# Kernel tuning notes

Hardware: AMD Instinct MI355X
Metric: run time of the kernel (lower is better)

## Reference

```python
import jax, jax.numpy as jnp
import numpy as np

EPS = 1e-8
Q_MAX = 127.0  # 2**(8-1) - 1


def _activation_quant(x):
    gamma = jnp.maximum(jnp.max(jnp.abs(x)), EPS)
    scale = Q_MAX / gamma
    x_int = jnp.clip(jnp.round(x * scale), -Q_MAX, Q_MAX)
    x_fq = x_int / scale
    # straight-through estimator
    return x + jax.lax.stop_gradient(x_fq - x)


def _weight_quant(w):
    gamma = jnp.maximum(jnp.mean(jnp.abs(w)), EPS)
    w_int = jnp.clip(jnp.round(w / gamma), -1.0, 1.0)
    w_fq = w_int * gamma
    return w + jax.lax.stop_gradient(w_fq - w)


def setup_inputs() -> dict:
    key = jax.random.key(0)
    kx, kw, kb = jax.random.split(key, 3)
    in_features, out_features = 2048, 2048
    x = jax.random.normal(kx, (4, 4096, in_features), dtype=jnp.float32)
    # nn.Linear default init: U(-1/sqrt(fan_in), 1/sqrt(fan_in))
    bound = 1.0 / np.sqrt(in_features)
    W = jax.random.uniform(kw, (out_features, in_features), dtype=jnp.float32,
                           minval=-bound, maxval=bound)
    b = jax.random.uniform(kb, (out_features,), dtype=jnp.float32,
                           minval=-bound, maxval=bound)
    return {"x": x, "W": W, "b": b}


def reference(x, W, b):
    x_q = _activation_quant(x)          # int8 absmax fake-quant
    w_q = _weight_quant(W)              # ternary {-g, 0, g} fake-quant
    # F.linear: x @ W^T + b
    return jnp.einsum('bsi,oi->bso', x_q, w_q) + b
```

## Files before the change

### kernel.cpp

```cpp
#include <hip/hip_runtime.h>
#include <hip/hip_bf16.h>
#include <stdint.h>

typedef __attribute__((ext_vector_type(4))) int i32x4;

static constexpr long M_ = 16384;
static constexpr long N_ = 2048;
static constexpr long K_ = 2048;


#define GLOAD_LDS16(g, l)                                                          \
  __builtin_amdgcn_global_load_lds(                                               \
      (const __attribute__((address_space(1))) unsigned int*)(g),                 \
      (__attribute__((address_space(3))) unsigned int*)(l), 16, 0, 0)

__global__ __launch_bounds__(256) void k_stats(const float4* __restrict__ x,
                                               const float4* __restrict__ w,
                                               unsigned* __restrict__ gx_bits,
                                               double* __restrict__ gw_sum) {
  const int b = blockIdx.x;
  const int lane = threadIdx.x & 63, wv = threadIdx.x >> 6;
  if (b < 2048) {
    const long S = 524288;
    long i = (long)b * 256 + threadIdx.x;
    float m0 = 0.f, m1 = 0.f;
#pragma unroll
    for (int it = 0; it < 8; ++it) {
      float4 v0 = x[i];
      float4 v1 = x[i + S];
      m0 = fmaxf(m0, fmaxf(fmaxf(fabsf(v0.x), fabsf(v0.y)), fmaxf(fabsf(v0.z), fabsf(v0.w))));
      m1 = fmaxf(m1, fmaxf(fmaxf(fabsf(v1.x), fabsf(v1.y)), fmaxf(fabsf(v1.z), fabsf(v1.w))));
      i += 2 * S;
    }
    float m = fmaxf(m0, m1);
#pragma unroll
    for (int off = 32; off > 0; off >>= 1) m = fmaxf(m, __shfl_down(m, off));
    __shared__ float sm[4];
    if (lane == 0) sm[wv] = m;
    __syncthreads();
    if (threadIdx.x == 0) {
      float bm = fmaxf(fmaxf(sm[0], sm[1]), fmaxf(sm[2], sm[3]));
      atomicMax(gx_bits, __float_as_uint(bm));
    }
  } else {
    const long S = 131072;
    long i = (long)(b - 2048) * 256 + threadIdx.x;
    double s = 0.0;
#pragma unroll
    for (int it = 0; it < 8; ++it) {
      float4 v = w[i];
      s += (double)fabsf(v.x) + (double)fabsf(v.y) + (double)fabsf(v.z) + (double)fabsf(v.w);
      i += S;
    }
#pragma unroll
    for (int off = 32; off > 0; off >>= 1) s += __shfl_down(s, off);
    __shared__ double sd[4];
    if (lane == 0) sd[wv] = s;
    __syncthreads();
    if (threadIdx.x == 0) atomicAdd(gw_sum, (sd[0] + sd[1]) + (sd[2] + sd[3]));
  }
}

__global__ __launch_bounds__(256) void k_quant(const float4* __restrict__ x,
                                               const float4* __restrict__ w,
                                               char4* __restrict__ xq,
                                               char4* __restrict__ wq,
                                               const unsigned* __restrict__ gx_bits,
                                               const double* __restrict__ gw_sum) {
  const int b = blockIdx.x;
  if (b < 2048) {
    const double gx = (double)fmaxf(__uint_as_float(*gx_bits), 1e-8f);
    const double scale = 127.0 / gx;
    const long S = 524288;
    long i = (long)b * 256 + threadIdx.x;
#pragma unroll
    for (int it = 0; it < 16; ++it) {
      float4 v = x[i];
      char4 o;
      o.x = (signed char)(int)fmin(fmax(rint((double)v.x * scale), -127.0), 127.0);
      o.y = (signed char)(int)fmin(fmax(rint((double)v.y * scale), -127.0), 127.0);
      o.z = (signed char)(int)fmin(fmax(rint((double)v.z * scale), -127.0), 127.0);
      o.w = (signed char)(int)fmin(fmax(rint((double)v.w * scale), -127.0), 127.0);
      xq[i] = o;
      i += S;
    }
  } else {
    const double gw = fmax(*gw_sum * (1.0 / 4194304.0), 1e-8);
    const double inv = 1.0 / gw;
    const long S = 131072;
    long i = (long)(b - 2048) * 256 + threadIdx.x;
#pragma unroll
    for (int it = 0; it < 8; ++it) {
      float4 v = w[i];
      char4 o;
      o.x = (signed char)(int)fmin(fmax(rint((double)v.x * inv), -1.0), 1.0);
      o.y = (signed char)(int)fmin(fmax(rint((double)v.y * inv), -1.0), 1.0);
      o.z = (signed char)(int)fmin(fmax(rint((double)v.z * inv), -1.0), 1.0);
      o.w = (signed char)(int)fmin(fmax(rint((double)v.w * inv), -1.0), 1.0);
      wq[i] = o;
      i += S;
    }
  }
}


template <int ISB, int BUF, int KS>
__device__ __forceinline__ void stage2(signed char* lds, const signed char* gp, int kb,
                                       int go0, int ldsl0) {
  constexpr int R = ISB * 65536 + BUF * 32768 + KS * 16384;
  GLOAD_LDS16(gp + kb + go0, lds + R + ldsl0);
  GLOAD_LDS16(gp + kb + go0 + 32768, lds + R + ldsl0 + 1024);
}

template <int BUF, int KS, int SGBUF, int SGKS>
__device__ __forceinline__ void pairphase(signed char* lds, const signed char* Ap,
                                          const signed char* Bp, int kb,
                                          const signed char* pA, const signed char* pB,
                                          int go0, int ldsl0, i32x4 acc[8][4]) {
  constexpr int RB = BUF * 32768 + KS * 16384;
  i32x4 b4[4], alo[4], ahi[4];
#pragma unroll
  for (int n = 0; n < 4; ++n) b4[n] = *(const i32x4*)(pB + RB + n * 1024);
#pragma unroll
  for (int m = 0; m < 4; ++m) alo[m] = *(const i32x4*)(pA + RB + m * 1024);
#pragma unroll
  for (int m = 0; m < 4; ++m) ahi[m] = *(const i32x4*)(pA + RB + 4096 + m * 1024);

  stage2<0, SGBUF, SGKS>(lds, Ap, kb, go0, ldsl0);
  stage2<1, SGBUF, SGKS>(lds, Bp, kb, go0, ldsl0);

  __builtin_amdgcn_s_barrier();
  __builtin_amdgcn_s_setprio(1);
#pragma unroll
  for (int m = 0; m < 4; ++m)
#pragma unroll
    for (int n = 0; n < 4; ++n)
      acc[m][n] = __builtin_amdgcn_mfma_i32_16x16x64_i8(alo[m], b4[n], acc[m][n], 0, 0, 0);
#pragma unroll
  for (int m = 0; m < 4; ++m)
#pragma unroll
    for (int n = 0; n < 4; ++n)
      acc[4 + m][n] =
          __builtin_amdgcn_mfma_i32_16x16x64_i8(ahi[m], b4[n], acc[4 + m][n], 0, 0, 0);
  __builtin_amdgcn_s_setprio(0);
  asm volatile("s_waitcnt vmcnt(8)" ::: "memory");
  __builtin_amdgcn_s_barrier();
  __builtin_amdgcn_sched_barrier(0);
}

__global__ __launch_bounds__(512, 2) void k_gemm(
    const signed char* __restrict__ Aq, const signed char* __restrict__ Bq,
    const float* __restrict__ bias, float* __restrict__ out,
    const unsigned* __restrict__ gx_bits, const double* __restrict__ gw_sum) {
  extern __shared__ signed char lds[];

  const int tid = threadIdx.x;
  const int lane = tid & 63;
  const int wid = tid >> 6;
  const int wave_m = wid >> 2;
  const int wave_n = wid & 3;
  const int l15 = lane & 15;

  const int wg = (int)((blockIdx.x & 7) * 64 + (blockIdx.x >> 3));
  const int nblk = wg & 7;
  const int mblk = wg >> 3;
  const long brow = (long)mblk * 256;
  const long bcol = (long)nblk * 256;

  const signed char* Ap = Aq + brow * K_;
  const signed char* Bp = Bq + bcol * K_;

  const int swz = ((lane >> 4) ^ ((l15 >> 1) & 3)) << 4;
  const signed char* pA = lds + (wave_m * 128 + l15) * 64 + swz;
  const signed char* pB = lds + 65536 + (wave_n * 64 + l15) * 64 + swz;

  const int c0 = (lane & 3) ^ ((lane >> 3) & 3);
  const int go0 = (wid * 32 + (lane >> 2)) * (int)K_ + c0 * 16;
  const int ldsl0 = wid * 2048;

  i32x4 acc[8][4];
#pragma unroll
  for (int m = 0; m < 8; m++)
#pragma unroll
    for (int n = 0; n < 4; n++) acc[m][n] = (i32x4){0, 0, 0, 0};

  stage2<0, 0, 0>(lds, Ap, 0, go0, ldsl0);
  stage2<1, 0, 0>(lds, Bp, 0, go0, ldsl0);
  stage2<0, 0, 1>(lds, Ap, 64, go0, ldsl0);
  stage2<1, 0, 1>(lds, Bp, 64, go0, ldsl0);
  stage2<0, 1, 0>(lds, Ap, 128, go0, ldsl0);
  stage2<1, 1, 0>(lds, Bp, 128, go0, ldsl0);
  asm volatile("s_waitcnt vmcnt(0)" ::: "memory");
  __builtin_amdgcn_s_barrier();

  for (int kt = 0; kt < (int)K_; kt += 256) {
    const int k1h = (kt + 192) & 2047;
    const int k2 = (kt + 256) & 2047;
    const int k3 = (kt + 384) & 2047;
    pairphase<0, 0, 1, 1>(lds, Ap, Bp, k1h, pA, pB, go0, ldsl0, acc);
    pairphase<0, 1, 0, 0>(lds, Ap, Bp, k2, pA, pB, go0, ldsl0, acc);
    pairphase<1, 0, 0, 1>(lds, Ap, Bp, k2 + 64, pA, pB, go0, ldsl0, acc);
    pairphase<1, 1, 1, 0>(lds, Ap, Bp, k3, pA, pB, go0, ldsl0, acc);
  }

  const float gxf = fmaxf(__uint_as_float(*gx_bits), 1e-8f);
  const double gwd = fmax(*gw_sum * (1.0 / 4194304.0), 1e-8);
  const float alpha = (float)((double)gxf * gwd * (1.0 / 127.0));

#pragma unroll
  for (int n = 0; n < 4; ++n) {
    const long col = bcol + wave_n * 64 + n * 16 + l15;
    const float bv = bias[col];
#pragma unroll
    for (int m = 0; m < 8; ++m) {
      const long row0 = brow + wave_m * 128 + m * 16 + (lane >> 4) * 4;
#pragma unroll
      for (int r = 0; r < 4; ++r) {
        out[(row0 + r) * N_ + col] = (float)acc[m][n][r] * alpha + bv;
      }
    }
  }
}

extern "C" void kernel_launch(void* const* d_in, const int* in_sizes, int n_in,
                              void* d_out, int out_size, void* d_ws, size_t ws_size,
                              hipStream_t stream) {
  const float* x = (const float*)d_in[0];
  const float* W = (const float*)d_in[1];
  const float* b = (const float*)d_in[2];
  float* out = (float*)d_out;

  char* ws = (char*)d_ws;
  double* gw_sum = (double*)ws;
  unsigned* gx_bits = (unsigned*)(ws + 8);
  signed char* xq = (signed char*)(ws + 256);
  signed char* wq = (signed char*)(ws + 256 + (size_t)M_ * (size_t)K_);

  static bool attr_set = false;
  if (!attr_set) {
    (void)hipFuncSetAttribute(reinterpret_cast<const void*>(&k_gemm),
                              hipFuncAttributeMaxDynamicSharedMemorySize, 131072);
    attr_set = true;
  }

  hipMemsetAsync(ws, 0, 16, stream);
  hipLaunchKernelGGL(k_stats, dim3(2560), dim3(256), 0, stream,
                     (const float4*)x, (const float4*)W, gx_bits, gw_sum);
  hipLaunchKernelGGL(k_quant, dim3(2560), dim3(256), 0, stream,
                     (const float4*)x, (const float4*)W, (char4*)xq, (char4*)wq,
                     gx_bits, gw_sum);
  hipLaunchKernelGGL(k_gemm, dim3((unsigned)((M_ / 256) * (N_ / 256))), dim3(512),
                     131072, stream, xq, wq, b, out, gx_bits, gw_sum);
}
```

Baseline: 155.7 us.

## Shrink GEMM tile to 128x256 with 4 waves and double-buffered LDS

The int8 GEMM moves from a 256x256 tile with 8 waves and 128 KB of LDS in a deep 4-slot pipeline to a 128x256 tile with 4 waves, 48 KB of LDS and a simple two-buffer scheme. A and B prefetches are split across the two MFMA halves of each k-step. The smaller LDS footprint and block should allow more resident workgroups and give a finer grid, at the cost of less operand reuse per tile and a full vmcnt(0) wait every k-step. The stats kernel also unrolls its absmax loop to four independent loads per iteration.

New measurement: 158.3 us. About the same (+1.6%).

```diff
diff --git a/kernel.cpp b/kernel.cpp
--- a/kernel.cpp
+++ b/kernel.cpp
@@ -23,16 +23,20 @@
   if (b < 2048) {
     const long S = 524288;
     long i = (long)b * 256 + threadIdx.x;
-    float m0 = 0.f, m1 = 0.f;
-#pragma unroll
-    for (int it = 0; it < 8; ++it) {
+    float m0 = 0.f, m1 = 0.f, m2 = 0.f, m3 = 0.f;
+#pragma unroll
+    for (int it = 0; it < 4; ++it) {
       float4 v0 = x[i];
       float4 v1 = x[i + S];
+      float4 v2 = x[i + 2 * S];
+      float4 v3 = x[i + 3 * S];
       m0 = fmaxf(m0, fmaxf(fmaxf(fabsf(v0.x), fabsf(v0.y)), fmaxf(fabsf(v0.z), fabsf(v0.w))));
       m1 = fmaxf(m1, fmaxf(fmaxf(fabsf(v1.x), fabsf(v1.y)), fmaxf(fabsf(v1.z), fabsf(v1.w))));
-      i += 2 * S;
-    }
-    float m = fmaxf(m0, m1);
+      m2 = fmaxf(m2, fmaxf(fmaxf(fabsf(v2.x), fabsf(v2.y)), fmaxf(fabsf(v2.z), fabsf(v2.w))));
+      m3 = fmaxf(m3, fmaxf(fmaxf(fabsf(v3.x), fabsf(v3.y)), fmaxf(fabsf(v3.z), fabsf(v3.w))));
+      i += 4 * S;
+    }
+    float m = fmaxf(fmaxf(m0, m1), fmaxf(m2, m3));
 #pragma unroll
     for (int off = 32; off > 0; off >>= 1) m = fmaxf(m, __shfl_down(m, off));
     __shared__ float sm[4];
@@ -104,51 +108,65 @@
 }
 
 
-template <int ISB, int BUF, int KS>
-__device__ __forceinline__ void stage2(signed char* lds, const signed char* gp, int kb,
-                                       int go0, int ldsl0) {
-  constexpr int R = ISB * 65536 + BUF * 32768 + KS * 16384;
-  GLOAD_LDS16(gp + kb + go0, lds + R + ldsl0);
-  GLOAD_LDS16(gp + kb + go0 + 32768, lds + R + ldsl0 + 1024);
-}
-
-template <int BUF, int KS, int SGBUF, int SGKS>
-__device__ __forceinline__ void pairphase(signed char* lds, const signed char* Ap,
-                                          const signed char* Bp, int kb,
-                                          const signed char* pA, const signed char* pB,
-                                          int go0, int ldsl0, i32x4 acc[8][4]) {
-  constexpr int RB = BUF * 32768 + KS * 16384;
-  i32x4 b4[4], alo[4], ahi[4];
+template <int BUF>
+__device__ __forceinline__ void stageA(signed char* lds, const signed char* gp, int kb,
+                                       int goA, int wslotA) {
+  constexpr int R = BUF * 8192;
+  GLOAD_LDS16(gp + kb + goA, lds + R + wslotA);
+  GLOAD_LDS16(gp + kb + goA + 16 * 2048, lds + R + wslotA + 1024);
+}
+
+template <int BUF>
+__device__ __forceinline__ void stageB(signed char* lds, const signed char* gp, int kb,
+                                       int goB, int wslotB) {
+  constexpr int R = 16384 + BUF * 16384;
+  GLOAD_LDS16(gp + kb + goB, lds + R + wslotB);
+  GLOAD_LDS16(gp + kb + goB + 16 * 2048, lds + R + wslotB + 1024);
+  GLOAD_LDS16(gp + kb + goB + 32 * 2048, lds + R + wslotB + 2048);
+  GLOAD_LDS16(gp + kb + goB + 48 * 2048, lds + R + wslotB + 3072);
+}
+
+template <int C>
+__device__ __forceinline__ void kstep(signed char* lds, const signed char* Ap,
+                                      const signed char* Bp, int kb,
+                                      const signed char* pA, const signed char* pB,
+                                      int goA, int goB, int wslotA, int wslotB,
+                                      i32x4 acc[8][4]) {
+  constexpr int RA = C * 8192;
+  constexpr int RB = 16384 + C * 16384;
+  i32x4 b4[4], a4[4];
 #pragma unroll
   for (int n = 0; n < 4; ++n) b4[n] = *(const i32x4*)(pB + RB + n * 1024);
 #pragma unroll
-  for (int m = 0; m < 4; ++m) alo[m] = *(const i32x4*)(pA + RB + m * 1024);
-#pragma unroll
-  for (int m = 0; m < 4; ++m) ahi[m] = *(const i32x4*)(pA + RB + 4096 + m * 1024);
-
-  stage2<0, SGBUF, SGKS>(lds, Ap, kb, go0, ldsl0);
-  stage2<1, SGBUF, SGKS>(lds, Bp, kb, go0, ldsl0);
-
-  __builtin_amdgcn_s_barrier();
+  for (int m = 0; m < 4; ++m) a4[m] = *(const i32x4*)(pA + RA + m * 1024);
+  stageA<C ^ 1>(lds, Ap, kb, goA, wslotA);
+  __builtin_amdgcn_s_barrier();
+  asm volatile("s_waitcnt lgkmcnt(0)" ::: "memory");
   __builtin_amdgcn_s_setprio(1);
 #pragma unroll
   for (int m = 0; m < 4; ++m)
 #pragma unroll
     for (int n = 0; n < 4; ++n)
-      acc[m][n] = __builtin_amdgcn_mfma_i32_16x16x64_i8(alo[m], b4[n], acc[m][n], 0, 0, 0);
+      acc[m][n] = __builtin_amdgcn_mfma_i32_16x16x64_i8(a4[m], b4[n], acc[m][n], 0, 0, 0);
+  __builtin_amdgcn_s_setprio(0);
+#pragma unroll
+  for (int m = 0; m < 4; ++m) a4[m] = *(const i32x4*)(pA + RA + 4096 + m * 1024);
+  stageB<C ^ 1>(lds, Bp, kb, goB, wslotB);
+  __builtin_amdgcn_s_barrier();
+  asm volatile("s_waitcnt lgkmcnt(0)" ::: "memory");
+  __builtin_amdgcn_s_setprio(1);
 #pragma unroll
   for (int m = 0; m < 4; ++m)
 #pragma unroll
     for (int n = 0; n < 4; ++n)
       acc[4 + m][n] =
-          __builtin_amdgcn_mfma_i32_16x16x64_i8(ahi[m], b4[n], acc[4 + m][n], 0, 0, 0);
+          __builtin_amdgcn_mfma_i32_16x16x64_i8(a4[m], b4[n], acc[4 + m][n], 0, 0, 0);
   __builtin_amdgcn_s_setprio(0);
-  asm volatile("s_waitcnt vmcnt(8)" ::: "memory");
-  __builtin_amdgcn_s_barrier();
-  __builtin_amdgcn_sched_barrier(0);
-}
-
-__global__ __launch_bounds__(512, 2) void k_gemm(
+  asm volatile("s_waitcnt vmcnt(0)" ::: "memory");
+  __builtin_amdgcn_s_barrier();
+}
+
+__global__ __launch_bounds__(256, 2) void k_gemm(
     const signed char* __restrict__ Aq, const signed char* __restrict__ Bq,
     const float* __restrict__ bias, float* __restrict__ out,
     const unsigned* __restrict__ gx_bits, const double* __restrict__ gw_sum) {
@@ -157,26 +175,26 @@
   const int tid = threadIdx.x;
   const int lane = tid & 63;
   const int wid = tid >> 6;
-  const int wave_m = wid >> 2;
-  const int wave_n = wid & 3;
   const int l15 = lane & 15;
 
-  const int wg = (int)((blockIdx.x & 7) * 64 + (blockIdx.x >> 3));
+  const int wg = (int)((blockIdx.x & 7) * 128 + (blockIdx.x >> 3));
   const int nblk = wg & 7;
   const int mblk = wg >> 3;
-  const long brow = (long)mblk * 256;
+  const long brow = (long)mblk * 128;
   const long bcol = (long)nblk * 256;
 
   const signed char* Ap = Aq + brow * K_;
   const signed char* Bp = Bq + bcol * K_;
 
   const int swz = ((lane >> 4) ^ ((l15 >> 1) & 3)) << 4;
-  const signed char* pA = lds + (wave_m * 128 + l15) * 64 + swz;
-  const signed char* pB = lds + 65536 + (wave_n * 64 + l15) * 64 + swz;
+  const signed char* pA = lds + l15 * 64 + swz;
+  const signed char* pB = lds + (wid * 64 + l15) * 64 + swz;
 
   const int c0 = (lane & 3) ^ ((lane >> 3) & 3);
-  const int go0 = (wid * 32 + (lane >> 2)) * (int)K_ + c0 * 16;
-  const int ldsl0 = wid * 2048;
+  const int goA = (wid * 32 + (lane >> 2)) * (int)K_ + c0 * 16;
+  const int goB = (wid * 64 + (lane >> 2)) * (int)K_ + c0 * 16;
+  const int wslotA = wid * 2048;
+  const int wslotB = wid * 4096;
 
   i32x4 acc[8][4];
 #pragma unroll
@@ -184,23 +202,16 @@
 #pragma unroll
     for (int n = 0; n < 4; n++) acc[m][n] = (i32x4){0, 0, 0, 0};
 
-  stage2<0, 0, 0>(lds, Ap, 0, go0, ldsl0);
-  stage2<1, 0, 0>(lds, Bp, 0, go0, ldsl0);
-  stage2<0, 0, 1>(lds, Ap, 64, go0, ldsl0);
-  stage2<1, 0, 1>(lds, Bp, 64, go0, ldsl0);
-  stage2<0, 1, 0>(lds, Ap, 128, go0, ldsl0);
-  stage2<1, 1, 0>(lds, Bp, 128, go0, ldsl0);
+  stageA<0>(lds, Ap, 0, goA, wslotA);
+  stageB<0>(lds, Bp, 0, goB, wslotB);
   asm volatile("s_waitcnt vmcnt(0)" ::: "memory");
   __builtin_amdgcn_s_barrier();
 
-  for (int kt = 0; kt < (int)K_; kt += 256) {
-    const int k1h = (kt + 192) & 2047;
-    const int k2 = (kt + 256) & 2047;
-    const int k3 = (kt + 384) & 2047;
-    pairphase<0, 0, 1, 1>(lds, Ap, Bp, k1h, pA, pB, go0, ldsl0, acc);
-    pairphase<0, 1, 0, 0>(lds, Ap, Bp, k2, pA, pB, go0, ldsl0, acc);
-    pairphase<1, 0, 0, 1>(lds, Ap, Bp, k2 + 64, pA, pB, go0, ldsl0, acc);
-    pairphase<1, 1, 1, 0>(lds, Ap, Bp, k3, pA, pB, go0, ldsl0, acc);
+  for (int kt = 0; kt < (int)K_; kt += 128) {
+    const int kb0 = kt + 64;
+    const int kb1 = (kt + 128) & 2047;
+    kstep<0>(lds, Ap, Bp, kb0, pA, pB, goA, goB, wslotA, wslotB, acc);
+    kstep<1>(lds, Ap, Bp, kb1, pA, pB, goA, goB, wslotA, wslotB, acc);
   }
 
   const float gxf = fmaxf(__uint_as_float(*gx_bits), 1e-8f);
@@ -209,11 +220,11 @@
 
 #pragma unroll
   for (int n = 0; n < 4; ++n) {
-    const long col = bcol + wave_n * 64 + n * 16 + l15;
+    const long col = bcol + wid * 64 + n * 16 + l15;
     const float bv = bias[col];
 #pragma unroll
     for (int m = 0; m < 8; ++m) {
-      const long row0 = brow + wave_m * 128 + m * 16 + (lane >> 4) * 4;
+      const long row0 = brow + m * 16 + (lane >> 4) * 4;
 #pragma unroll
       for (int r = 0; r < 4; ++r) {
         out[(row0 + r) * N_ + col] = (float)acc[m][n][r] * alpha + bv;
@@ -236,19 +247,12 @@
   signed char* xq = (signed char*)(ws + 256);
   signed char* wq = (signed char*)(ws + 256 + (size_t)M_ * (size_t)K_);
 
-  static bool attr_set = false;
-  if (!attr_set) {
-    (void)hipFuncSetAttribute(reinterpret_cast<const void*>(&k_gemm),
-                              hipFuncAttributeMaxDynamicSharedMemorySize, 131072);
-    attr_set = true;
-  }
-
   hipMemsetAsync(ws, 0, 16, stream);
   hipLaunchKernelGGL(k_stats, dim3(2560), dim3(256), 0, stream,
                      (const float4*)x, (const float4*)W, gx_bits, gw_sum);
   hipLaunchKernelGGL(k_quant, dim3(2560), dim3(256), 0, stream,
                      (const float4*)x, (const float4*)W, (char4*)xq, (char4*)wq,
                      gx_bits, gw_sum);
-  hipLaunchKernelGGL(k_gemm, dim3((unsigned)((M_ / 256) * (N_ / 256))), dim3(512),
-                     131072, stream, xq, wq, b, out, gx_bits, gw_sum);
-}
+  hipLaunchKernelGGL(k_gemm, dim3((unsigned)((M_ / 128) * (N_ / 256))), dim3(256),
+                     49152, stream, xq, wq, b, out, gx_bits, gw_sum);
+}
```

## Restructure GEMM main loop into eight half-phases with register double-buffered LDS fragments

Applied to the files above, without the earlier changes.

The int8 GEMM main loop now runs eight finer phases per 256-wide K step instead of four. Each phase preloads the next phase's A and B fragments from LDS into a second register buffer before issuing its own MFMAs, and the global-to-LDS staging is split so A and B loads alternate across phases. This lets LDS reads overlap MFMA work instead of sitting in front of it, at the cost of more barriers and extra registers for the double buffer. The stats kernel's x absmax loop is also unrolled to four independent loads per iteration for more memory-level parallelism.

After: 155.9 us. No clear change (+0.1%).

```diff
diff --git a/kernel.cpp b/kernel.cpp
--- a/kernel.cpp
+++ b/kernel.cpp
@@ -23,16 +23,20 @@
   if (b < 2048) {
     const long S = 524288;
     long i = (long)b * 256 + threadIdx.x;
-    float m0 = 0.f, m1 = 0.f;
-#pragma unroll
-    for (int it = 0; it < 8; ++it) {
+    float m0 = 0.f, m1 = 0.f, m2 = 0.f, m3 = 0.f;
+#pragma unroll
+    for (int it = 0; it < 4; ++it) {
       float4 v0 = x[i];
       float4 v1 = x[i + S];
+      float4 v2 = x[i + 2 * S];
+      float4 v3 = x[i + 3 * S];
       m0 = fmaxf(m0, fmaxf(fmaxf(fabsf(v0.x), fabsf(v0.y)), fmaxf(fabsf(v0.z), fabsf(v0.w))));
       m1 = fmaxf(m1, fmaxf(fmaxf(fabsf(v1.x), fabsf(v1.y)), fmaxf(fabsf(v1.z), fabsf(v1.w))));
-      i += 2 * S;
-    }
-    float m = fmaxf(m0, m1);
+      m2 = fmaxf(m2, fmaxf(fmaxf(fabsf(v2.x), fabsf(v2.y)), fmaxf(fabsf(v2.z), fabsf(v2.w))));
+      m3 = fmaxf(m3, fmaxf(fmaxf(fabsf(v3.x), fabsf(v3.y)), fmaxf(fabsf(v3.z), fabsf(v3.w))));
+      i += 4 * S;
+    }
+    float m = fmaxf(fmaxf(m0, m1), fmaxf(m2, m3));
 #pragma unroll
     for (int off = 32; off > 0; off >>= 1) m = fmaxf(m, __shfl_down(m, off));
     __shared__ float sm[4];
@@ -104,48 +108,46 @@
 }
 
 
-template <int ISB, int BUF, int KS>
-__device__ __forceinline__ void stage2(signed char* lds, const signed char* gp, int kb,
-                                       int go0, int ldsl0) {
-  constexpr int R = ISB * 65536 + BUF * 32768 + KS * 16384;
-  GLOAD_LDS16(gp + kb + go0, lds + R + ldsl0);
-  GLOAD_LDS16(gp + kb + go0 + 32768, lds + R + ldsl0 + 1024);
-}
-
-template <int BUF, int KS, int SGBUF, int SGKS>
-__device__ __forceinline__ void pairphase(signed char* lds, const signed char* Ap,
-                                          const signed char* Bp, int kb,
-                                          const signed char* pA, const signed char* pB,
-                                          int go0, int ldsl0, i32x4 acc[8][4]) {
-  constexpr int RB = BUF * 32768 + KS * 16384;
-  i32x4 b4[4], alo[4], ahi[4];
-#pragma unroll
-  for (int n = 0; n < 4; ++n) b4[n] = *(const i32x4*)(pB + RB + n * 1024);
-#pragma unroll
-  for (int m = 0; m < 4; ++m) alo[m] = *(const i32x4*)(pA + RB + m * 1024);
-#pragma unroll
-  for (int m = 0; m < 4; ++m) ahi[m] = *(const i32x4*)(pA + RB + 4096 + m * 1024);
-
-  stage2<0, SGBUF, SGKS>(lds, Ap, kb, go0, ldsl0);
-  stage2<1, SGBUF, SGKS>(lds, Bp, kb, go0, ldsl0);
-
+template <int P>
+__device__ __forceinline__ void phaseP(signed char* lds, const signed char* Ap,
+                                       const signed char* Bp, int kb,
+                                       const signed char* pA, const signed char* pB,
+                                       int go0, int ldsl0, i32x4 (&aS)[2][4],
+                                       i32x4 (&bS)[2][4], i32x4 (&acc)[8][4]) {
+  constexpr int Q = (P + 1) & 7;
+  constexpr int QR = ((Q >> 2) & 1) * 32768 + ((Q >> 1) & 1) * 16384;
+  constexpr int QMH = Q & 1;
+#pragma unroll
+  for (int m = 0; m < 4; ++m)
+    aS[Q & 1][m] = *(const i32x4*)(pA + QR + QMH * 4096 + m * 1024);
+  if constexpr (QMH == 0) {
+#pragma unroll
+    for (int n = 0; n < 4; ++n)
+      bS[(Q >> 1) & 1][n] = *(const i32x4*)(pB + QR + n * 1024);
+  }
+  __builtin_amdgcn_sched_barrier(0);
+  constexpr int SREG = ((P >> 1) + 3) & 3;
+  constexpr int SOFF = ((SREG >> 1) & 1) * 32768 + (SREG & 1) * 16384;
+  if constexpr ((P & 1) == 0) {
+    GLOAD_LDS16(Ap + kb + go0, lds + SOFF + ldsl0);
+    GLOAD_LDS16(Ap + kb + go0 + 32768, lds + SOFF + ldsl0 + 1024);
+  } else {
+    GLOAD_LDS16(Bp + kb + go0, lds + 65536 + SOFF + ldsl0);
+    GLOAD_LDS16(Bp + kb + go0 + 32768, lds + 65536 + SOFF + ldsl0 + 1024);
+  }
+  __builtin_amdgcn_sched_barrier(0);
+  __builtin_amdgcn_s_setprio(1);
+#pragma unroll
+  for (int m = 0; m < 4; ++m)
+#pragma unroll
+    for (int n = 0; n < 4; ++n)
+      acc[(P & 1) * 4 + m][n] = __builtin_amdgcn_mfma_i32_16x16x64_i8(
+          aS[P & 1][m], bS[(P >> 1) & 1][n], acc[(P & 1) * 4 + m][n], 0, 0, 0);
+  __builtin_amdgcn_s_setprio(0);
+  asm volatile("s_waitcnt lgkmcnt(0)" ::: "memory");
+  __builtin_amdgcn_sched_barrier(0);
+  if constexpr ((P & 1) == 1) asm volatile("s_waitcnt vmcnt(4)" ::: "memory");
   __builtin_amdgcn_s_barrier();
-  __builtin_amdgcn_s_setprio(1);
-#pragma unroll
-  for (int m = 0; m < 4; ++m)
-#pragma unroll
-    for (int n = 0; n < 4; ++n)
-      acc[m][n] = __builtin_amdgcn_mfma_i32_16x16x64_i8(alo[m], b4[n], acc[m][n], 0, 0, 0);
-#pragma unroll
-  for (int m = 0; m < 4; ++m)
-#pragma unroll
-    for (int n = 0; n < 4; ++n)
-      acc[4 + m][n] =
-          __builtin_amdgcn_mfma_i32_16x16x64_i8(ahi[m], b4[n], acc[4 + m][n], 0, 0, 0);
-  __builtin_amdgcn_s_setprio(0);
-  asm volatile("s_waitcnt vmcnt(8)" ::: "memory");
-  __builtin_amdgcn_s_barrier();
-  __builtin_amdgcn_sched_barrier(0);
 }
 
 __global__ __launch_bounds__(512, 2) void k_gemm(
@@ -183,24 +185,43 @@
   for (int m = 0; m < 8; m++)
 #pragma unroll
     for (int n = 0; n < 4; n++) acc[m][n] = (i32x4){0, 0, 0, 0};
-
-  stage2<0, 0, 0>(lds, Ap, 0, go0, ldsl0);
-  stage2<1, 0, 0>(lds, Bp, 0, go0, ldsl0);
-  stage2<0, 0, 1>(lds, Ap, 64, go0, ldsl0);
-  stage2<1, 0, 1>(lds, Bp, 64, go0, ldsl0);
-  stage2<0, 1, 0>(lds, Ap, 128, go0, ldsl0);
-  stage2<1, 1, 0>(lds, Bp, 128, go0, ldsl0);
+  i32x4 aS[2][4], bS[2][4];
+
+  GLOAD_LDS16(Ap + go0, lds + ldsl0);
+  GLOAD_LDS16(Ap + go0 + 32768, lds + ldsl0 + 1024);
+  GLOAD_LDS16(Bp + go0, lds + 65536 + ldsl0);
+  GLOAD_LDS16(Bp + go0 + 32768, lds + 65536 + ldsl0 + 1024);
+  GLOAD_LDS16(Ap + 64 + go0, lds + 16384 + ldsl0);
+  GLOAD_LDS16(Ap + 64 + go0 + 32768, lds + 16384 + ldsl0 + 1024);
+  GLOAD_LDS16(Bp + 64 + go0, lds + 65536 + 16384 + ldsl0);
+  GLOAD_LDS16(Bp + 64 + go0 + 32768, lds + 65536 + 16384 + ldsl0 + 1024);
+  GLOAD_LDS16(Ap + 128 + go0, lds + 32768 + ldsl0);
+  GLOAD_LDS16(Ap + 128 + go0 + 32768, lds + 32768 + ldsl0 + 1024);
+  GLOAD_LDS16(Bp + 128 + go0, lds + 65536 + 32768 + ldsl0);
+  GLOAD_LDS16(Bp + 128 + go0 + 32768, lds + 65536 + 32768 + ldsl0 + 1024);
   asm volatile("s_waitcnt vmcnt(0)" ::: "memory");
   __builtin_amdgcn_s_barrier();
 
+#pragma unroll
+  for (int n = 0; n < 4; ++n) bS[0][n] = *(const i32x4*)(pB + n * 1024);
+#pragma unroll
+  for (int m = 0; m < 4; ++m) aS[0][m] = *(const i32x4*)(pA + m * 1024);
+  asm volatile("s_waitcnt lgkmcnt(0)" ::: "memory");
+  __builtin_amdgcn_sched_barrier(0);
+
   for (int kt = 0; kt < (int)K_; kt += 256) {
-    const int k1h = (kt + 192) & 2047;
-    const int k2 = (kt + 256) & 2047;
-    const int k3 = (kt + 384) & 2047;
-    pairphase<0, 0, 1, 1>(lds, Ap, Bp, k1h, pA, pB, go0, ldsl0, acc);
-    pairphase<0, 1, 0, 0>(lds, Ap, Bp, k2, pA, pB, go0, ldsl0, acc);
-    pairphase<1, 0, 0, 1>(lds, Ap, Bp, k2 + 64, pA, pB, go0, ldsl0, acc);
-    pairphase<1, 1, 1, 0>(lds, Ap, Bp, k3, pA, pB, go0, ldsl0, acc);
+    const int c0k = (kt + 192) & 2047;
+    const int c1k = (kt + 256) & 2047;
+    const int c2k = (kt + 320) & 2047;
+    const int c3k = (kt + 384) & 2047;
+    phaseP<0>(lds, Ap, Bp, c0k, pA, pB, go0, ldsl0, aS, bS, acc);
+    phaseP<1>(lds, Ap, Bp, c0k, pA, pB, go0, ldsl0, aS, bS, acc);
+    phaseP<2>(lds, Ap, Bp, c1k, pA, pB, go0, ldsl0, aS, bS, acc);
+    phaseP<3>(lds, Ap, Bp, c1k, pA, pB, go0, ldsl0, aS, bS, acc);
+    phaseP<4>(lds, Ap, Bp, c2k, pA, pB, go0, ldsl0, aS, bS, acc);
+    phaseP<5>(lds, Ap, Bp, c2k, pA, pB, go0, ldsl0, aS, bS, acc);
+    phaseP<6>(lds, Ap, Bp, c3k, pA, pB, go0, ldsl0, aS, bS, acc);
+    phaseP<7>(lds, Ap, Bp, c3k, pA, pB, go0, ldsl0, aS, bS, acc);
   }
 
   const float gxf = fmaxf(__uint_as_float(*gx_bits), 1e-8f);
```
